# Performance work log

Measured on AMD Instinct MI355X. Metric: run time of the kernel, lower is better.

## Reference

```python
import jax, jax.numpy as jnp
import numpy as np

VOCAB, D = 100000, 128
B, V, L = 2048, 50, 20
N_CLASS = 128

def setup_inputs() -> dict:
    key = jax.random.key(0)
    k1, k2, k3, k4, k5 = jax.random.split(key, 5)
    return {
        "diag_idx": jax.random.randint(k1, (B, V, L), 0, VOCAB),
        "proc_idx": jax.random.randint(k2, (B, V, L), 0, VOCAB),
        "emb": jax.random.normal(k3, (VOCAB, D), dtype=jnp.float32),
        "W": jax.random.normal(k4, (N_CLASS, 2 * D), dtype=jnp.float32) * 0.05,
        "b": jax.random.normal(k5, (N_CLASS,), dtype=jnp.float32) * 0.05,
    }

def _pool(emb, idx):
    # gather [B,V,L,D], mean over codes (dim=1 in torch per-sample == axis 2 here),
    # then sum over visits (dim=0 per-sample == axis 1 here) -> [B, D]
    g = emb[idx]
    return g.mean(axis=2).sum(axis=1)

def reference(diag_idx, proc_idx, emb, W, b):
    d = _pool(emb, diag_idx)            # [B, D]
    p = _pool(emb, proc_idx)            # [B, D]
    x = jnp.concatenate([d, p], axis=-1)  # [B, 2D]
    return x @ W.T + b                  # [B, n_class]
```

## Files before the change

kernel.cpp:

```cpp
#include <hip/hip_runtime.h>


typedef _Float16 h2 __attribute__((ext_vector_type(2)));

constexpr int B      = 2048;
constexpr int V      = 50;
constexpr int L      = 20;
constexpr int D      = 128;
constexpr int NIDX   = V * L;
constexpr int NCLASS = 128;
constexpr int TWO_D  = 2 * D;
constexpr int VOCAB  = 100000;
constexpr int NSLICE = 8;
constexpr int SLICE_ROWS = VOCAB / NSLICE;
constexpr int SROWS_P    = SLICE_ROWS + 1;

__device__ __forceinline__ unsigned short f2bf_rne(float f) {
    unsigned int u = __float_as_uint(f);
    unsigned int r = (u + 0x7FFFu + ((u >> 16) & 1u)) >> 16;
    return (unsigned short)r;
}
__device__ __forceinline__ float uif(unsigned int u) { return __uint_as_float(u); }

__device__ __forceinline__ unsigned int pk_f16(float a, float b) {
    return __builtin_bit_cast(unsigned int, __builtin_amdgcn_cvt_pkrtz(a, b));
}
__device__ __forceinline__ h2 h2_shfl_xor(h2 a, int m) {
    return __builtin_bit_cast(h2, __shfl_xor(__builtin_bit_cast(int, a), m, 64));
}

__global__ __launch_bounds__(256)
void prep_kernel(const float* __restrict__ emb,
                 const int* __restrict__ diag_idx,
                 const int* __restrict__ proc_idx,
                 unsigned short* __restrict__ embb,
                 unsigned short* __restrict__ sorted,
                 int* __restrict__ offs)
{
    const int bid = blockIdx.x;
    const int tid = threadIdx.x;

    if (bid < 12500) {
        const int i4 = bid * 256 + tid;
        const int r  = i4 >> 5;
        const int s  = r / SLICE_ROWS;
        const float4 v = reinterpret_cast<const float4*>(emb)[i4];
        uint2 o;
        o.x = pk_f16(v.x, v.y);
        o.y = pk_f16(v.z, v.w);
        reinterpret_cast<uint2*>(embb)[i4 + s * 32] = o;
        return;
    }
    if (bid == 12500) {
        const int s = tid >> 5, u = tid & 31;
        reinterpret_cast<uint2*>(embb)[((size_t)s * SROWS_P + SLICE_ROWS) * 32 + u] =
            make_uint2(0u, 0u);
        return;
    }

    const int b = bid - 12501;

    __shared__ int cnt[2][NSLICE];
    __shared__ int woff[2][NSLICE];
    __shared__ int offsS[2][NSLICE + 1];
    __shared__ unsigned short sl[2][NIDX];

    if (tid < 16) cnt[tid >> 3][tid & 7] = 0;
    __syncthreads();

    int4 qd = make_int4(0, 0, 0, 0), qp = make_int4(0, 0, 0, 0);
    const bool act = tid < NIDX / 4;
    if (act) {
        qd = reinterpret_cast<const int4*>(diag_idx + (size_t)b * NIDX)[tid];
        qp = reinterpret_cast<const int4*>(proc_idx + (size_t)b * NIDX)[tid];
        atomicAdd(&cnt[0][qd.x / SLICE_ROWS], 1);
        atomicAdd(&cnt[0][qd.y / SLICE_ROWS], 1);
        atomicAdd(&cnt[0][qd.z / SLICE_ROWS], 1);
        atomicAdd(&cnt[0][qd.w / SLICE_ROWS], 1);
        atomicAdd(&cnt[1][qp.x / SLICE_ROWS], 1);
        atomicAdd(&cnt[1][qp.y / SLICE_ROWS], 1);
        atomicAdd(&cnt[1][qp.z / SLICE_ROWS], 1);
        atomicAdd(&cnt[1][qp.w / SLICE_ROWS], 1);
    }
    __syncthreads();

    if (tid < 2) {
        int run = 0;
        for (int k = 0; k < NSLICE; ++k) {
            offsS[tid][k] = run;
            woff[tid][k]  = run;
            run += cnt[tid][k];
        }
        offsS[tid][NSLICE] = run;
    }
    __syncthreads();

    if (act) {
        int s, p;
        s = qd.x / SLICE_ROWS; p = atomicAdd(&woff[0][s], 1); sl[0][p] = (unsigned short)(qd.x - s * SLICE_ROWS);
        s = qd.y / SLICE_ROWS; p = atomicAdd(&woff[0][s], 1); sl[0][p] = (unsigned short)(qd.y - s * SLICE_ROWS);
        s = qd.z / SLICE_ROWS; p = atomicAdd(&woff[0][s], 1); sl[0][p] = (unsigned short)(qd.z - s * SLICE_ROWS);
        s = qd.w / SLICE_ROWS; p = atomicAdd(&woff[0][s], 1); sl[0][p] = (unsigned short)(qd.w - s * SLICE_ROWS);
        s = qp.x / SLICE_ROWS; p = atomicAdd(&woff[1][s], 1); sl[1][p] = (unsigned short)(qp.x - s * SLICE_ROWS);
        s = qp.y / SLICE_ROWS; p = atomicAdd(&woff[1][s], 1); sl[1][p] = (unsigned short)(qp.y - s * SLICE_ROWS);
        s = qp.z / SLICE_ROWS; p = atomicAdd(&woff[1][s], 1); sl[1][p] = (unsigned short)(qp.z - s * SLICE_ROWS);
        s = qp.w / SLICE_ROWS; p = atomicAdd(&woff[1][s], 1); sl[1][p] = (unsigned short)(qp.w - s * SLICE_ROWS);
    }
    __syncthreads();

    unsigned int* so = reinterpret_cast<unsigned int*>(sorted + (size_t)b * 2 * NIDX);
    for (int t = tid; t < NIDX; t += 256) {
        const int h = t / (NIDX / 2), i = t % (NIDX / 2);
        so[t] = (unsigned int)sl[h][2 * i] | ((unsigned int)sl[h][2 * i + 1] << 16);
    }
    if (tid < 2 * (NSLICE + 1))
        offs[b * 2 * (NSLICE + 1) + tid] = offsS[tid / (NSLICE + 1)][tid % (NSLICE + 1)];
}

__global__ __launch_bounds__(256, 6)
void slice_pool_kernel(const unsigned short* __restrict__ embb,
                       const unsigned short* __restrict__ sorted,
                       const int* __restrict__ offs,
                       unsigned int* __restrict__ pooledp)
{
    const int bid  = blockIdx.x;
    const int s    = bid & (NSLICE - 1);
    const int bq   = bid >> 3;
    const int tid  = threadIdx.x;
    const int wave = tid >> 6;
    const int lane = tid & 63;
    const int b    = bq * 2 + (wave >> 1);
    const int h    = wave & 1;

    const int* ob  = offs + (b * 2 + h) * (NSLICE + 1);
    const int beg  = ob[s];
    const int n    = ob[s + 1] - beg;

    const unsigned short* __restrict__ lst =
        sorted + (size_t)(b * 2 + h) * NIDX + beg;
    const uint4* __restrict__ sbase =
        reinterpret_cast<const uint4*>(embb + (size_t)s * SROWS_P * D);

    const int sub = lane >> 4;
    const int c   = lane & 15;

    h2 a0 = {0, 0}, a1 = {0, 0}, a2 = {0, 0}, a3 = {0, 0};
    #pragma unroll 8
    for (int i = 0; i < n; i += 4) {
        const int j  = i + sub;
        const int rv = (int)lst[j];
        const int rl = (j < n) ? rv : SLICE_ROWS;
        const uint4 e = sbase[rl * 16 + c];
        a0 += __builtin_bit_cast(h2, e.x);
        a1 += __builtin_bit_cast(h2, e.y);
        a2 += __builtin_bit_cast(h2, e.z);
        a3 += __builtin_bit_cast(h2, e.w);
    }

    a0 += h2_shfl_xor(a0, 16); a1 += h2_shfl_xor(a1, 16);
    a2 += h2_shfl_xor(a2, 16); a3 += h2_shfl_xor(a3, 16);
    a0 += h2_shfl_xor(a0, 32); a1 += h2_shfl_xor(a1, 32);
    a2 += h2_shfl_xor(a2, 32); a3 += h2_shfl_xor(a3, 32);

    if (lane < 16) {
        uint4 o;
        o.x = __builtin_bit_cast(unsigned int, a0);
        o.y = __builtin_bit_cast(unsigned int, a1);
        o.z = __builtin_bit_cast(unsigned int, a2);
        o.w = __builtin_bit_cast(unsigned int, a3);
        reinterpret_cast<uint4*>(pooledp + ((size_t)((b * 2 + h) * NSLICE + s) * 64))[c] = o;
    }
}

__global__ __launch_bounds__(128)
void head_kernel(const unsigned int* __restrict__ pooledp,
                 const float* __restrict__ W,
                 const float* __restrict__ bias,
                 float* __restrict__ out)
{
    __shared__ float x[TWO_D];
    const int b   = blockIdx.x;
    const int tid = threadIdx.x;
    const int h   = tid >> 6;
    const int c2  = tid & 63;

    const unsigned int* pp = pooledp + (size_t)(b * 2 + h) * NSLICE * 64 + c2;
    float sx = 0.f, sy = 0.f;
    #pragma unroll
    for (int sl = 0; sl < NSLICE; ++sl) {
        const h2 v = __builtin_bit_cast(h2, pp[sl * 64]);
        sx += (float)v.x;
        sy += (float)v.y;
    }
    x[h * D + 2 * c2]     = sx * (1.0f / L);
    x[h * D + 2 * c2 + 1] = sy * (1.0f / L);
    __syncthreads();

    const float4* __restrict__ wrow =
        reinterpret_cast<const float4*>(W + (size_t)tid * TWO_D);
    const float4* __restrict__ xv = reinterpret_cast<const float4*>(x);
    float acc = bias[tid];
    #pragma unroll 16
    for (int k = 0; k < TWO_D / 4; ++k) {
        const float4 w4 = wrow[k];
        const float4 x4 = xv[k];
        acc = fmaf(w4.x, x4.x, acc);
        acc = fmaf(w4.y, x4.y, acc);
        acc = fmaf(w4.z, x4.z, acc);
        acc = fmaf(w4.w, x4.w, acc);
    }
    out[(size_t)b * NCLASS + tid] = acc;
}

__global__ __launch_bounds__(256)
void convert_flat_kernel(const float* __restrict__ emb, unsigned short* __restrict__ o)
{
    const int i = blockIdx.x * 256 + threadIdx.x;
    const float4 v = reinterpret_cast<const float4*>(emb)[i];
    ushort4 u;
    u.x = f2bf_rne(v.x); u.y = f2bf_rne(v.y);
    u.z = f2bf_rne(v.z); u.w = f2bf_rne(v.w);
    reinterpret_cast<ushort4*>(o)[i] = u;
}

__global__ __launch_bounds__(256, 4)
void pool_gemm_bf16_kernel(const int* __restrict__ diag_idx,
                           const int* __restrict__ proc_idx,
                           const unsigned short* __restrict__ embb,
                           const float* __restrict__ W,
                           const float* __restrict__ bias,
                           float* __restrict__ out)
{
    __shared__ float4 part4[4][64];
    __shared__ float  x_lds[TWO_D];

    const int b    = blockIdx.x;
    const int tid  = threadIdx.x;
    const int wave = tid >> 6;
    const int lane = tid & 63;

    const int half  = wave >> 1;
    const int chunk = wave & 1;
    const int* __restrict__ idx =
        (half == 0 ? diag_idx : proc_idx) + (size_t)b * NIDX + (size_t)chunk * (NIDX / 2);
    const int2* __restrict__ idx2 = reinterpret_cast<const int2*>(idx);

    const ushort4* __restrict__ emb4 = reinterpret_cast<const ushort4*>(embb);
    const int c = lane & 31;

    float4 acc = make_float4(0.f, 0.f, 0.f, 0.f);
    #pragma unroll 10
    for (int i = 0; i < NIDX / 4; ++i) {
        const int2 p = idx2[i];
        const int  r = (lane & 32) ? p.y : p.x;
        const ushort4 e = emb4[(size_t)r * (D / 4) + c];
        acc.x += uif((unsigned int)e.x << 16);
        acc.y += uif((unsigned int)e.y << 16);
        acc.z += uif((unsigned int)e.z << 16);
        acc.w += uif((unsigned int)e.w << 16);
    }
    part4[wave][lane] = acc;
    __syncthreads();

    {
        const int h   = tid >> 7;
        const int rem = tid & 127;
        const int cc  = rem >> 2;
        const int j   = rem & 3;
        const float* p0 = reinterpret_cast<const float*>(&part4[2 * h][cc]);
        const float* p1 = reinterpret_cast<const float*>(&part4[2 * h][cc + 32]);
        const float* p2 = reinterpret_cast<const float*>(&part4[2 * h + 1][cc]);
        const float* p3 = reinterpret_cast<const float*>(&part4[2 * h + 1][cc + 32]);
        x_lds[tid] = (p0[j] + p1[j] + p2[j] + p3[j]) * (1.0f / L);
    }
    __syncthreads();

    if (tid < NCLASS) {
        const float4* __restrict__ wrow =
            reinterpret_cast<const float4*>(W + (size_t)tid * TWO_D);
        const float4* __restrict__ xv = reinterpret_cast<const float4*>(x_lds);
        float s = bias[tid];
        #pragma unroll 8
        for (int k = 0; k < TWO_D / 4; ++k) {
            const float4 w4 = wrow[k];
            const float4 x4 = xv[k];
            s = fmaf(w4.x, x4.x, s);
            s = fmaf(w4.y, x4.y, s);
            s = fmaf(w4.z, x4.z, s);
            s = fmaf(w4.w, x4.w, s);
        }
        out[(size_t)b * NCLASS + tid] = s;
    }
}

__global__ __launch_bounds__(256, 4)
void pool_gemm_f32_kernel(const int* __restrict__ diag_idx,
                          const int* __restrict__ proc_idx,
                          const float* __restrict__ emb,
                          const float* __restrict__ W,
                          const float* __restrict__ bias,
                          float* __restrict__ out)
{
    __shared__ float4 part4[4][64];
    __shared__ float  x_lds[TWO_D];

    const int b    = blockIdx.x;
    const int tid  = threadIdx.x;
    const int wave = tid >> 6;
    const int lane = tid & 63;

    const int half  = wave >> 1;
    const int chunk = wave & 1;
    const int* __restrict__ idx =
        (half == 0 ? diag_idx : proc_idx) + (size_t)b * NIDX + (size_t)chunk * (NIDX / 2);
    const int2* __restrict__ idx2 = reinterpret_cast<const int2*>(idx);

    const float4* __restrict__ emb4 = reinterpret_cast<const float4*>(emb);
    const int c = lane & 31;

    float4 acc = make_float4(0.f, 0.f, 0.f, 0.f);
    #pragma unroll 5
    for (int i = 0; i < NIDX / 4; ++i) {
        const int2 p = idx2[i];
        const int  r = (lane & 32) ? p.y : p.x;
        const float4 e = emb4[(size_t)r * (D / 4) + c];
        acc.x += e.x; acc.y += e.y; acc.z += e.z; acc.w += e.w;
    }
    part4[wave][lane] = acc;
    __syncthreads();

    {
        const int h   = tid >> 7;
        const int rem = tid & 127;
        const int cc  = rem >> 2;
        const int j   = rem & 3;
        const float* p0 = reinterpret_cast<const float*>(&part4[2 * h][cc]);
        const float* p1 = reinterpret_cast<const float*>(&part4[2 * h][cc + 32]);
        const float* p2 = reinterpret_cast<const float*>(&part4[2 * h + 1][cc]);
        const float* p3 = reinterpret_cast<const float*>(&part4[2 * h + 1][cc + 32]);
        x_lds[tid] = (p0[j] + p1[j] + p2[j] + p3[j]) * (1.0f / L);
    }
    __syncthreads();

    if (tid < NCLASS) {
        const float4* __restrict__ wrow =
            reinterpret_cast<const float4*>(W + (size_t)tid * TWO_D);
        const float4* __restrict__ xv = reinterpret_cast<const float4*>(x_lds);
        float s = bias[tid];
        #pragma unroll 8
        for (int k = 0; k < TWO_D / 4; ++k) {
            const float4 w4 = wrow[k];
            const float4 x4 = xv[k];
            s = fmaf(w4.x, x4.x, s);
            s = fmaf(w4.y, x4.y, s);
            s = fmaf(w4.z, x4.z, s);
            s = fmaf(w4.w, x4.w, s);
        }
        out[(size_t)b * NCLASS + tid] = s;
    }
}

extern "C" void kernel_launch(void* const* d_in, const int* in_sizes, int n_in,
                              void* d_out, int out_size, void* d_ws, size_t ws_size,
                              hipStream_t stream)
{
    const int*   diag = (const int*)d_in[0];
    const int*   proc = (const int*)d_in[1];
    const float* emb  = (const float*)d_in[2];
    const float* W    = (const float*)d_in[3];
    const float* bias = (const float*)d_in[4];
    float*       out  = (float*)d_out;

    const size_t embb_bytes    = (size_t)NSLICE * SROWS_P * D * sizeof(unsigned short);
    const size_t sorted_bytes  = (size_t)B * 2 * NIDX * sizeof(unsigned short) + 16;
    const size_t offs_bytes    = (size_t)B * 2 * (NSLICE + 1) * sizeof(int);
    const size_t pooledp_bytes = (size_t)B * 2 * NSLICE * 64 * sizeof(unsigned int);
    const size_t need = embb_bytes + sorted_bytes + offs_bytes + pooledp_bytes;

    const size_t emb_flat_bytes = (size_t)VOCAB * D * sizeof(unsigned short);

    if (ws_size >= need) {
        char* p = (char*)d_ws;
        unsigned short* embb    = (unsigned short*)p;             p += embb_bytes;
        unsigned short* sorted  = (unsigned short*)p;             p += sorted_bytes;
        int*            offs    = (int*)p;                        p += offs_bytes;
        unsigned int*   pooledp = (unsigned int*)p;

        prep_kernel<<<12501 + B, 256, 0, stream>>>(emb, diag, proc, embb, sorted, offs);
        slice_pool_kernel<<<(B / 2) * NSLICE, 256, 0, stream>>>(embb, sorted, offs, pooledp);
        head_kernel<<<B, 128, 0, stream>>>(pooledp, W, bias, out);
    } else if (ws_size >= emb_flat_bytes) {
        unsigned short* embb = (unsigned short*)d_ws;
        convert_flat_kernel<<<(VOCAB * D / 4) / 256, 256, 0, stream>>>(emb, embb);
        pool_gemm_bf16_kernel<<<B, 256, 0, stream>>>(diag, proc, embb, W, bias, out);
    } else {
        pool_gemm_f32_kernel<<<B, 256, 0, stream>>>(diag, proc, emb, W, bias, out);
    }
}
```

Before: 185.4 us.

## Bucket indices per wave with ballot counting and pad slices to multiples of four

After: 198.1 us. 1.07x slower.

```diff
diff --git a/kernel.cpp b/kernel.cpp
--- a/kernel.cpp
+++ b/kernel.cpp
@@ -14,6 +14,7 @@
 constexpr int NSLICE = 8;
 constexpr int SLICE_ROWS = VOCAB / NSLICE;
 constexpr int SROWS_P    = SLICE_ROWS + 1;
+constexpr int LCAP       = 1024;
 
 __device__ __forceinline__ unsigned short f2bf_rne(float f) {
     unsigned int u = __float_as_uint(f);
@@ -37,6 +38,8 @@
                  unsigned short* __restrict__ sorted,
                  int* __restrict__ offs)
 {
+    __shared__ unsigned short lst_s[4][LCAP];
+
     const int bid = blockIdx.x;
     const int tid = threadIdx.x;
 
@@ -58,63 +61,90 @@
         return;
     }
 
-    const int b = bid - 12501;
-
-    __shared__ int cnt[2][NSLICE];
-    __shared__ int woff[2][NSLICE];
-    __shared__ int offsS[2][NSLICE + 1];
-    __shared__ unsigned short sl[2][NIDX];
-
-    if (tid < 16) cnt[tid >> 3][tid & 7] = 0;
-    __syncthreads();
-
-    int4 qd = make_int4(0, 0, 0, 0), qp = make_int4(0, 0, 0, 0);
-    const bool act = tid < NIDX / 4;
-    if (act) {
-        qd = reinterpret_cast<const int4*>(diag_idx + (size_t)b * NIDX)[tid];
-        qp = reinterpret_cast<const int4*>(proc_idx + (size_t)b * NIDX)[tid];
-        atomicAdd(&cnt[0][qd.x / SLICE_ROWS], 1);
-        atomicAdd(&cnt[0][qd.y / SLICE_ROWS], 1);
-        atomicAdd(&cnt[0][qd.z / SLICE_ROWS], 1);
-        atomicAdd(&cnt[0][qd.w / SLICE_ROWS], 1);
-        atomicAdd(&cnt[1][qp.x / SLICE_ROWS], 1);
-        atomicAdd(&cnt[1][qp.y / SLICE_ROWS], 1);
-        atomicAdd(&cnt[1][qp.z / SLICE_ROWS], 1);
-        atomicAdd(&cnt[1][qp.w / SLICE_ROWS], 1);
-    }
-    __syncthreads();
-
-    if (tid < 2) {
-        int run = 0;
-        for (int k = 0; k < NSLICE; ++k) {
-            offsS[tid][k] = run;
-            woff[tid][k]  = run;
-            run += cnt[tid][k];
+    const int bq   = bid - 12501;
+    const int wave = tid >> 6;
+    const int lane = tid & 63;
+    const int b    = bq * 2 + (wave >> 1);
+    const int h    = wave & 1;
+    const int* __restrict__ ig = (h ? proc_idx : diag_idx) + (size_t)b * NIDX;
+
+    int4 q[4];
+    #pragma unroll
+    for (int t = 0; t < 4; ++t) {
+        const int i4 = t * 64 + lane;
+        q[t] = (i4 < NIDX / 4) ? reinterpret_cast<const int4*>(ig)[i4]
+                               : make_int4(-1, -1, -1, -1);
+    }
+
+    int cnt[NSLICE];
+    #pragma unroll
+    for (int k = 0; k < NSLICE; ++k) cnt[k] = 0;
+    #pragma unroll
+    for (int t = 0; t < 4; ++t) {
+        const int vv[4] = {q[t].x, q[t].y, q[t].z, q[t].w};
+        #pragma unroll
+        for (int c = 0; c < 4; ++c) {
+            const unsigned s = (unsigned)vv[c] / (unsigned)SLICE_ROWS;
+            #pragma unroll
+            for (int k = 0; k < NSLICE; ++k)
+                cnt[k] += (int)__popcll(__ballot(s == (unsigned)k));
         }
-        offsS[tid][NSLICE] = run;
-    }
-    __syncthreads();
-
-    if (act) {
-        int s, p;
-        s = qd.x / SLICE_ROWS; p = atomicAdd(&woff[0][s], 1); sl[0][p] = (unsigned short)(qd.x - s * SLICE_ROWS);
-        s = qd.y / SLICE_ROWS; p = atomicAdd(&woff[0][s], 1); sl[0][p] = (unsigned short)(qd.y - s * SLICE_ROWS);
-        s = qd.z / SLICE_ROWS; p = atomicAdd(&woff[0][s], 1); sl[0][p] = (unsigned short)(qd.z - s * SLICE_ROWS);
-        s = qd.w / SLICE_ROWS; p = atomicAdd(&woff[0][s], 1); sl[0][p] = (unsigned short)(qd.w - s * SLICE_ROWS);
-        s = qp.x / SLICE_ROWS; p = atomicAdd(&woff[1][s], 1); sl[1][p] = (unsigned short)(qp.x - s * SLICE_ROWS);
-        s = qp.y / SLICE_ROWS; p = atomicAdd(&woff[1][s], 1); sl[1][p] = (unsigned short)(qp.y - s * SLICE_ROWS);
-        s = qp.z / SLICE_ROWS; p = atomicAdd(&woff[1][s], 1); sl[1][p] = (unsigned short)(qp.z - s * SLICE_ROWS);
-        s = qp.w / SLICE_ROWS; p = atomicAdd(&woff[1][s], 1); sl[1][p] = (unsigned short)(qp.w - s * SLICE_ROWS);
-    }
-    __syncthreads();
-
-    unsigned int* so = reinterpret_cast<unsigned int*>(sorted + (size_t)b * 2 * NIDX);
-    for (int t = tid; t < NIDX; t += 256) {
-        const int h = t / (NIDX / 2), i = t % (NIDX / 2);
-        so[t] = (unsigned int)sl[h][2 * i] | ((unsigned int)sl[h][2 * i + 1] << 16);
-    }
-    if (tid < 2 * (NSLICE + 1))
-        offs[b * 2 * (NSLICE + 1) + tid] = offsS[tid / (NSLICE + 1)][tid % (NSLICE + 1)];
+    }
+
+    int cnt4[NSLICE], seg[NSLICE + 1];
+    seg[0] = 0;
+    #pragma unroll
+    for (int k = 0; k < NSLICE; ++k) {
+        cnt4[k] = (cnt[k] + 3) & ~3;
+        seg[k + 1] = seg[k] + cnt4[k];
+    }
+    int base[NSLICE];
+    #pragma unroll
+    for (int k = 0; k < NSLICE; ++k) base[k] = seg[k];
+
+    const unsigned long long below = (1ull << lane) - 1ull;
+    #pragma unroll
+    for (int t = 0; t < 4; ++t) {
+        const int vv[4] = {q[t].x, q[t].y, q[t].z, q[t].w};
+        #pragma unroll
+        for (int c = 0; c < 4; ++c) {
+            const int r = vv[c];
+            const unsigned s = (unsigned)r / (unsigned)SLICE_ROWS;
+            int pos = -1;
+            #pragma unroll
+            for (int k = 0; k < NSLICE; ++k) {
+                const unsigned long long m = __ballot(s == (unsigned)k);
+                if (s == (unsigned)k) pos = base[k] + (int)__popcll(m & below);
+                base[k] += (int)__popcll(m);
+            }
+            if (pos >= 0)
+                lst_s[wave][pos] = (unsigned short)(r - (int)s * SLICE_ROWS);
+        }
+    }
+
+    #pragma unroll
+    for (int k = 0; k < NSLICE; ++k) {
+        const int st = base[k];
+        if (lane < seg[k + 1] - st)
+            lst_s[wave][st + lane] = (unsigned short)SLICE_ROWS;
+    }
+
+    __syncthreads();
+
+    {
+        int val = 0;
+        #pragma unroll
+        for (int k = 1; k <= NSLICE; ++k)
+            val += (lane >= k) ? cnt4[k - 1] : 0;
+        if (lane < NSLICE + 1)
+            offs[(b * 2 + h) * (NSLICE + 1) + lane] = val;
+    }
+
+    const int tot = seg[NSLICE];
+    unsigned int* dst =
+        reinterpret_cast<unsigned int*>(sorted + (size_t)(b * 2 + h) * LCAP);
+    const unsigned int* src = reinterpret_cast<const unsigned int*>(&lst_s[wave][0]);
+    for (int i = lane; i < (tot >> 1); i += 64) dst[i] = src[i];
 }
 
 __global__ __launch_bounds__(256, 6)
@@ -134,10 +164,10 @@
 
     const int* ob  = offs + (b * 2 + h) * (NSLICE + 1);
     const int beg  = ob[s];
-    const int n    = ob[s + 1] - beg;
+    const int len  = ob[s + 1] - beg;
 
     const unsigned short* __restrict__ lst =
-        sorted + (size_t)(b * 2 + h) * NIDX + beg;
+        sorted + (size_t)(b * 2 + h) * LCAP + beg;
     const uint4* __restrict__ sbase =
         reinterpret_cast<const uint4*>(embb + (size_t)s * SROWS_P * D);
 
@@ -146,10 +176,8 @@
 
     h2 a0 = {0, 0}, a1 = {0, 0}, a2 = {0, 0}, a3 = {0, 0};
     #pragma unroll 8
-    for (int i = 0; i < n; i += 4) {
-        const int j  = i + sub;
-        const int rv = (int)lst[j];
-        const int rl = (j < n) ? rv : SLICE_ROWS;
+    for (int i = 0; i < len; i += 4) {
+        const int rl = (int)lst[i + sub];
         const uint4 e = sbase[rl * 16 + c];
         a0 += __builtin_bit_cast(h2, e.x);
         a1 += __builtin_bit_cast(h2, e.y);
@@ -372,7 +400,7 @@
     float*       out  = (float*)d_out;
 
     const size_t embb_bytes    = (size_t)NSLICE * SROWS_P * D * sizeof(unsigned short);
-    const size_t sorted_bytes  = (size_t)B * 2 * NIDX * sizeof(unsigned short) + 16;
+    const size_t sorted_bytes  = (size_t)B * 2 * LCAP * sizeof(unsigned short);
     const size_t offs_bytes    = (size_t)B * 2 * (NSLICE + 1) * sizeof(int);
     const size_t pooledp_bytes = (size_t)B * 2 * NSLICE * 64 * sizeof(unsigned int);
     const size_t need = embb_bytes + sorted_bytes + offs_bytes + pooledp_bytes;
@@ -386,7 +414,7 @@
         int*            offs    = (int*)p;                        p += offs_bytes;
         unsigned int*   pooledp = (unsigned int*)p;
 
-        prep_kernel<<<12501 + B, 256, 0, stream>>>(emb, diag, proc, embb, sorted, offs);
+        prep_kernel<<<12501 + B / 2, 256, 0, stream>>>(emb, diag, proc, embb, sorted, offs);
         slice_pool_kernel<<<(B / 2) * NSLICE, 256, 0, stream>>>(embb, sorted, offs, pooledp);
         head_kernel<<<B, 128, 0, stream>>>(pooledp, W, bias, out);
     } else if (ws_size >= emb_flat_bytes) {
```
